# Kernel optimization log

Measured on AMD Instinct MI355X. Metric: run time of the kernel, lower is better.

## Reference

```python
import jax, jax.numpy as jnp
import numpy as np


def setup_inputs() -> dict:
    key = jax.random.key(0)
    k1, k2 = jax.random.split(key)
    B, G, P = 64, 4999, 50
    raw_gene_expr = jax.random.normal(k1, (B, G), dtype=jnp.float32)
    # binary pathway membership matrix, mimics torch.randint(0, 2, (P, G)).float()
    pathway_gene_matrix = (jax.random.uniform(k2, (P, G)) < 0.5).astype(jnp.float32)
    return {"raw_gene_expr": raw_gene_expr, "pathway_gene_matrix": pathway_gene_matrix}


def reference(raw_gene_expr, pathway_gene_matrix):
    """Vectorized ssGSEA enrichment (compute_pathway_activations0).

    raw_gene_expr:        [B, G] float
    pathway_gene_matrix:  [P, G] binary float
    returns:              [B, P] signed max-deviation enrichment scores
    """
    B, G = raw_gene_expr.shape
    P = pathway_gene_matrix.shape[0]

    # Sort genes per sample in descending expression order
    order = jnp.argsort(-raw_gene_expr, axis=1)                      # [B, G]
    sorted_expr = jnp.take_along_axis(raw_gene_expr, order, axis=1)  # [B, G]

    # hit[b, p, i] = 1 if gene at sorted position i belongs to pathway p
    hit = (pathway_gene_matrix[:, order] > 0)                        # [P, B, G]
    hit = jnp.transpose(hit, (1, 0, 2)).astype(raw_gene_expr.dtype)  # [B, P, G]

    size = jnp.sum(pathway_gene_matrix > 0, axis=1).astype(raw_gene_expr.dtype)  # [P]

    # Weighted hit increments: |expr|^0.25 over hits, normalized per (sample, pathway)
    w = (jnp.abs(sorted_expr) ** 0.25)[:, None, :] * hit             # [B, P, G]
    s = jnp.sum(w, axis=-1, keepdims=True)
    w = jnp.where(s > 0, w / jnp.where(s > 0, s, 1.0), w)

    cum_hit = jnp.cumsum(w, axis=-1)                                 # [B, P, G]
    denom = jnp.maximum(G - size, 1.0)[None, :, None]                # guard size==G
    cum_miss = jnp.cumsum((1.0 - hit) / denom, axis=-1)              # [B, P, G]

    running = cum_hit - cum_miss                                     # [B, P, G]
    pos = jnp.argmax(jnp.abs(running), axis=-1)                      # [B, P]
    # signed max deviation == running value at the argmax of |running|
    es = jnp.take_along_axis(running, pos[..., None], axis=-1)[..., 0]  # [B, P]
    es = jnp.where(size[None, :] > 0, es, 0.0)
    return es
```

## Files before the change

### kernel.cpp

```cpp
#include <hip/hip_runtime.h>
#include <math.h>

typedef unsigned long long ull;

constexpr int Bc = 64;
constexpr int Gc = 4999;
constexpr int Pc = 50;

constexpr int RUN   = 512;
constexpr int NRUN  = 10;
constexpr int NPAD  = NRUN * RUN;
constexpr int EPT   = 8;
constexpr int LPW   = 79;
constexpr ull PADKEY = 0xFFFFFFFFFFFFFFFFull;

__device__ __forceinline__ ull shfl_xor64(ull v, int lm) {
    int lo = __shfl_xor((int)(unsigned)(v & 0xFFFFFFFFull), lm, 64);
    int hi = __shfl_xor((int)(unsigned)(v >> 32), lm, 64);
    return ((ull)(unsigned)hi << 32) | (unsigned)lo;
}

__global__ __launch_bounds__(1024) void sort_rank(
    const float* __restrict__ expr, const float* __restrict__ pathway,
    ull* __restrict__ pbits, float* __restrict__ wqout,
    unsigned short* __restrict__ sidxout, int G)
{
    __shared__ ull runsLDS[NPAD];
    const int rg = blockIdx.x, b = blockIdx.y;
    const int tid = threadIdx.x;
    const int lane = tid & 63;
    const int w = tid >> 6;

    if (w < NRUN) {
        const int base = lane * EPT;
        const float* row = expr + (size_t)b * G;
        ull v[EPT];
#pragma unroll
        for (int o = 0; o < EPT; ++o) {
            int i = w * RUN + base + o;
            if (i < G) {
                unsigned u = __float_as_uint(row[i]);
                unsigned m = (u >> 31) ? ~u : (u | 0x80000000u);
                v[o] = ((ull)(~m) << 32) | (unsigned)i;
            } else {
                v[o] = PADKEY;
            }
        }
#pragma unroll
        for (int kk = 2; kk <= RUN; kk <<= 1) {
#pragma unroll
            for (int j = kk >> 1; j >= EPT; j >>= 1) {
                const int lm = j >> 3;
                const bool takeMin = (((lane & lm) == 0) == ((base & kk) == 0));
#pragma unroll
                for (int o = 0; o < EPT; ++o) {
                    ull c = shfl_xor64(v[o], lm);
                    ull mn = (v[o] < c) ? v[o] : c;
                    ull mx = (v[o] < c) ? c : v[o];
                    v[o] = takeMin ? mn : mx;
                }
            }
#pragma unroll
            for (int j = 4; j >= 1; j >>= 1) {
                if (j < kk) {
#pragma unroll
                    for (int o = 0; o < EPT; ++o) {
                        if ((o & j) == 0) {
                            bool up = (((base + o) & kk) == 0);
                            ull a = v[o], c = v[o | j];
                            if ((a > c) == up) { v[o] = c; v[o | j] = a; }
                        }
                    }
                }
            }
        }
#pragma unroll
        for (int o = 0; o < EPT; ++o) runsLDS[w * RUN + base + o] = v[o];
    } else if (rg == 0) {
        for (int g = (w - NRUN) * 64 + lane; g < G; g += 6 * 64) {
        }
        int g = b * 384 + (w - NRUN) * 64 + lane;
        if (g < G) {
            ull m = 0;
#pragma unroll
            for (int p = 0; p < Pc; ++p)
                if (pathway[(size_t)p * G + g] > 0.0f) m |= (1ull << p);
            pbits[g] = m;
        }
    }
    __syncthreads();

    const int e = rg * 1024 + tid;
    const ull keyv = runsLDS[e];
    if (keyv == PADKEY) return;

    const int run = e >> 9;
    int rank = e & 511;
#pragma unroll
    for (int rr = 0; rr < NRUN; ++rr) {
        if (rr == run) continue;
        const ull* arr = &runsLDS[rr * RUN];
        int pos = 0;
#pragma unroll
        for (int s = RUN; s >= 1; s >>= 1) {
            int np = pos + s;
            if (np <= RUN && arr[np - 1] < keyv) pos = np;
        }
        rank += pos;
    }

    int idx = (int)(unsigned)(keyv & 0xFFFFFFFFu);
    unsigned m = ~((unsigned)(keyv >> 32));
    unsigned absbits = ((m >> 31) ? m : ~m) & 0x7FFFFFFFu;
    float av = __uint_as_float(absbits);
    wqout[(size_t)b * G + rank] = sqrtf(sqrtf(av));
    sidxout[(size_t)b * G + rank] = (unsigned short)idx;
}

__global__ __launch_bounds__(256) void es_kernel(
    const float* __restrict__ wq, const unsigned short* __restrict__ sidx,
    const ull* __restrict__ pbits, float* __restrict__ out, int B, int P, int G)
{
    __shared__ float    swq[Gc];
    __shared__ unsigned sm32[Gc];

    const int pg = blockIdx.x;
    const int b  = blockIdx.y;
    const int tid = threadIdx.x;
    const int pbeg = pg * 13;
    const int pend = (pbeg + 13 < P) ? (pbeg + 13) : P;

    for (int i = tid; i < G; i += 256) {
        swq[i]  = wq[(size_t)b * G + i];
        sm32[i] = (unsigned)(pbits[sidx[(size_t)b * G + i]] >> pbeg);
    }
    __syncthreads();

    const int lane = tid & 63;
    const int w = tid >> 6;
    const int p0 = pbeg + w * 4;
    if (p0 >= pend) return;
    const int sh4 = w * 4;

    const int start = lane * LPW;
    const int cnt = (start + LPW < G) ? LPW : (G - start);

    double sw[4] = {0.0, 0.0, 0.0, 0.0};
    int sh[4] = {0, 0, 0, 0};
    for (int k = 0; k < cnt; ++k) {
        int s = start + k;
        unsigned nib = (sm32[s] >> sh4) & 15u;
        double wv = (double)swq[s];
#pragma unroll
        for (int q = 0; q < 4; ++q) {
            if ((nib >> q) & 1u) { sw[q] += wv; sh[q]++; }
        }
    }
    double norm[4], inv_denom[4], running[4];
    int sht[4];
#pragma unroll
    for (int q = 0; q < 4; ++q) {
        double swt = sw[q];
        int shq = sh[q];
#pragma unroll
        for (int off = 1; off < 64; off <<= 1) {
            swt += __shfl_xor(swt, off, 64);
            shq += __shfl_xor(shq, off, 64);
        }
        sht[q] = shq;
        norm[q]      = (swt > 0.0) ? 1.0 / swt : 1.0;
        inv_denom[q] = 1.0 / fmax((double)(G - shq), 1.0);
        double csum = sw[q] * norm[q] - (double)(cnt - sh[q]) * inv_denom[q];
        double x = csum;
#pragma unroll
        for (int off = 1; off < 64; off <<= 1) {
            double vv = __shfl_up(x, off, 64);
            if (lane >= off) x += vv;
        }
        running[q] = x - csum;
    }

    double bestv[4] = {-1.0, -1.0, -1.0, -1.0};
    double bestr[4] = {0.0, 0.0, 0.0, 0.0};
    int besti[4] = {0x7FFFFFFF, 0x7FFFFFFF, 0x7FFFFFFF, 0x7FFFFFFF};
    for (int k = 0; k < cnt; ++k) {
        int s = start + k;
        unsigned nib = (sm32[s] >> sh4) & 15u;
        double wv = (double)swq[s];
#pragma unroll
        for (int q = 0; q < 4; ++q) {
            running[q] += ((nib >> q) & 1u) ? wv * norm[q] : -inv_denom[q];
            double a = fabs(running[q]);
            if (a > bestv[q]) { bestv[q] = a; bestr[q] = running[q]; besti[q] = s; }
        }
    }
#pragma unroll
    for (int q = 0; q < 4; ++q) {
#pragma unroll
        for (int off = 1; off < 64; off <<= 1) {
            double ov  = __shfl_xor(bestv[q], off, 64);
            double orr = __shfl_xor(bestr[q], off, 64);
            int    oi  = __shfl_xor(besti[q], off, 64);
            if (ov > bestv[q] || (ov == bestv[q] && oi < besti[q])) {
                bestv[q] = ov; bestr[q] = orr; besti[q] = oi;
            }
        }
    }

    if (lane == 0) {
#pragma unroll
        for (int q = 0; q < 4; ++q) {
            int p = p0 + q;
            if (p < pend)
                out[(size_t)b * P + p] = (sht[q] > 0) ? (float)bestr[q] : 0.0f;
        }
    }
}

extern "C" void kernel_launch(void* const* d_in, const int* in_sizes, int n_in,
                              void* d_out, int out_size, void* d_ws, size_t ws_size,
                              hipStream_t stream) {
    const float* expr    = (const float*)d_in[0];
    const float* pathway = (const float*)d_in[1];
    float* out = (float*)d_out;

    char* ws = (char*)d_ws;
    ull*            pbits = (ull*)ws;
    float*          wqa   = (float*)(ws + 40960);
    unsigned short* sidx  = (unsigned short*)(ws + 1320704);

    sort_rank<<<dim3(5, Bc), dim3(1024), 0, stream>>>(
        expr, pathway, pbits, wqa, sidx, Gc);
    es_kernel<<<dim3(4, Bc), dim3(256), 0, stream>>>(
        wqa, sidx, pbits, out, Bc, Pc, Gc);
}
```

Baseline: 127.5 us.

## Split sort into per-chunk sort kernel and separate rank-scatter merge kernel

The sorting stage is split into two kernels. The first sorts each 1024-element chunk in its own 256-thread block, using shared-memory passes for the large strides and shuffles for the rest, and writes the runs to global memory. A second kernel reloads all runs for a row and merges them by binary-search ranking across runs. Previously each of five blocks per sample re-sorted all ten runs redundantly. The split removes that duplicate sorting but adds a kernel launch and a global-memory round trip for the runs.

```diff
diff --git a/kernel.cpp b/kernel.cpp
--- a/kernel.cpp
+++ b/kernel.cpp
@@ -7,10 +7,9 @@
 constexpr int Gc = 4999;
 constexpr int Pc = 50;
 
-constexpr int RUN   = 512;
-constexpr int NRUN  = 10;
+constexpr int RUN   = 1024;
+constexpr int NRUN  = 5;
 constexpr int NPAD  = NRUN * RUN;
-constexpr int EPT   = 8;
 constexpr int LPW   = 79;
 constexpr ull PADKEY = 0xFFFFFFFFFFFFFFFFull;
 
@@ -20,66 +19,81 @@
     return ((ull)(unsigned)hi << 32) | (unsigned)lo;
 }
 
-__global__ __launch_bounds__(1024) void sort_rank(
+__global__ __launch_bounds__(256) void chunk_sort(
     const float* __restrict__ expr, const float* __restrict__ pathway,
-    ull* __restrict__ pbits, float* __restrict__ wqout,
-    unsigned short* __restrict__ sidxout, int G)
+    ull* __restrict__ runs, ull* __restrict__ pbits, int P, int G)
 {
-    __shared__ ull runsLDS[NPAD];
-    const int rg = blockIdx.x, b = blockIdx.y;
-    const int tid = threadIdx.x;
-    const int lane = tid & 63;
-    const int w = tid >> 6;
-
-    if (w < NRUN) {
-        const int base = lane * EPT;
-        const float* row = expr + (size_t)b * G;
-        ull v[EPT];
-#pragma unroll
-        for (int o = 0; o < EPT; ++o) {
-            int i = w * RUN + base + o;
-            if (i < G) {
-                unsigned u = __float_as_uint(row[i]);
-                unsigned m = (u >> 31) ? ~u : (u | 0x80000000u);
-                v[o] = ((ull)(~m) << 32) | (unsigned)i;
-            } else {
-                v[o] = PADKEY;
-            }
-        }
-#pragma unroll
-        for (int kk = 2; kk <= RUN; kk <<= 1) {
-#pragma unroll
-            for (int j = kk >> 1; j >= EPT; j >>= 1) {
-                const int lm = j >> 3;
-                const bool takeMin = (((lane & lm) == 0) == ((base & kk) == 0));
-#pragma unroll
-                for (int o = 0; o < EPT; ++o) {
-                    ull c = shfl_xor64(v[o], lm);
-                    ull mn = (v[o] < c) ? v[o] : c;
-                    ull mx = (v[o] < c) ? c : v[o];
-                    v[o] = takeMin ? mn : mx;
+    __shared__ ull key[RUN];
+    const int r = blockIdx.x, b = blockIdx.y, tid = threadIdx.x;
+    const int base = tid * 4;
+    const float* row = expr + (size_t)b * G;
+
+    ull v[4];
+#pragma unroll
+    for (int o = 0; o < 4; ++o) {
+        int i = r * RUN + base + o;
+        if (i < G) {
+            unsigned u = __float_as_uint(row[i]);
+            unsigned m = (u >> 31) ? ~u : (u | 0x80000000u);
+            v[o] = ((ull)(~m) << 32) | (unsigned)i;
+        } else {
+            v[o] = PADKEY;
+        }
+    }
+
+    for (int kk = 2; kk <= RUN; kk <<= 1) {
+        const int j0 = kk >> 1;
+        if (j0 >= 256) {
+#pragma unroll
+            for (int o = 0; o < 4; ++o) key[base + o] = v[o];
+            __syncthreads();
+            for (int j = j0; j >= 256; j >>= 1) {
+#pragma unroll
+                for (int t = tid; t < RUN / 2; t += 256) {
+                    int i  = ((t & ~(j - 1)) << 1) | (t & (j - 1));
+                    int ix = i | j;
+                    ull a = key[i], c = key[ix];
+                    bool up = ((i & kk) == 0);
+                    if ((a > c) == up) { key[i] = c; key[ix] = a; }
                 }
-            }
-#pragma unroll
-            for (int j = 4; j >= 1; j >>= 1) {
-                if (j < kk) {
-#pragma unroll
-                    for (int o = 0; o < EPT; ++o) {
-                        if ((o & j) == 0) {
-                            bool up = (((base + o) & kk) == 0);
-                            ull a = v[o], c = v[o | j];
-                            if ((a > c) == up) { v[o] = c; v[o | j] = a; }
-                        }
+                __syncthreads();
+            }
+#pragma unroll
+            for (int o = 0; o < 4; ++o) v[o] = key[base + o];
+        }
+        int jstart = (j0 > 128) ? 128 : j0;
+        for (int j = jstart; j >= 4; j >>= 1) {
+            int lm = j >> 2;
+            bool takeMin = (((tid & lm) == 0) == ((base & kk) == 0));
+#pragma unroll
+            for (int o = 0; o < 4; ++o) {
+                ull c = shfl_xor64(v[o], lm);
+                ull mn = (v[o] < c) ? v[o] : c;
+                ull mx = (v[o] < c) ? c : v[o];
+                v[o] = takeMin ? mn : mx;
+            }
+        }
+#pragma unroll
+        for (int j = 2; j >= 1; j >>= 1) {
+            if (j < kk) {
+#pragma unroll
+                for (int o = 0; o < 4; ++o) {
+                    if ((o & j) == 0) {
+                        bool up = (((base + o) & kk) == 0);
+                        ull a = v[o], c = v[o | j];
+                        if ((a > c) == up) { v[o] = c; v[o | j] = a; }
                     }
                 }
             }
         }
-#pragma unroll
-        for (int o = 0; o < EPT; ++o) runsLDS[w * RUN + base + o] = v[o];
-    } else if (rg == 0) {
-        for (int g = (w - NRUN) * 64 + lane; g < G; g += 6 * 64) {
-        }
-        int g = b * 384 + (w - NRUN) * 64 + lane;
+    }
+
+    ull* dst = runs + ((size_t)b * NRUN + r) * RUN;
+#pragma unroll
+    for (int o = 0; o < 4; ++o) dst[base + o] = v[o];
+
+    if (r == 0) {
+        int g = b * 256 + tid;
         if (g < G) {
             ull m = 0;
 #pragma unroll
@@ -88,14 +102,25 @@
             pbits[g] = m;
         }
     }
+}
+
+__global__ __launch_bounds__(1024) void rank_scatter(
+    const ull* __restrict__ runs,
+    float* __restrict__ wqout, unsigned short* __restrict__ sidxout, int G)
+{
+    __shared__ ull runsLDS[NPAD];
+    const int rg = blockIdx.x, b = blockIdx.y, tid = threadIdx.x;
+
+    const ull* rowruns = runs + (size_t)b * NPAD;
+    for (int i = tid; i < NPAD; i += 1024) runsLDS[i] = rowruns[i];
     __syncthreads();
 
     const int e = rg * 1024 + tid;
     const ull keyv = runsLDS[e];
     if (keyv == PADKEY) return;
 
-    const int run = e >> 9;
-    int rank = e & 511;
+    const int run = e >> 10;
+    int rank = e & 1023;
 #pragma unroll
     for (int rr = 0; rr < NRUN; ++rr) {
         if (rr == run) continue;
@@ -226,11 +251,13 @@
 
     char* ws = (char*)d_ws;
     ull*            pbits = (ull*)ws;
-    float*          wqa   = (float*)(ws + 40960);
-    unsigned short* sidx  = (unsigned short*)(ws + 1320704);
-
-    sort_rank<<<dim3(5, Bc), dim3(1024), 0, stream>>>(
-        expr, pathway, pbits, wqa, sidx, Gc);
+    ull*            runs  = (ull*)(ws + 40960);
+    float*          wqa   = (float*)(ws + 2662400);
+    unsigned short* sidx  = (unsigned short*)(ws + 3942144);
+
+    chunk_sort<<<dim3(NRUN, Bc), dim3(256), 0, stream>>>(
+        expr, pathway, runs, pbits, Pc, Gc);
+    rank_scatter<<<dim3(NRUN, Bc), dim3(1024), 0, stream>>>(runs, wqa, sidx, Gc);
     es_kernel<<<dim3(4, Bc), dim3(256), 0, stream>>>(
         wqa, sidx, pbits, out, Bc, Pc, Gc);
 }
```

After: 111.0 us. -12.9%, faster.
